# Optimization experiments

Measured on AMD Instinct MI355X. Metric: run time of the kernel, lower is better.

Reference implementation:

```python
import jax, jax.numpy as jnp
from jax import lax
import numpy as np

N = 262144   # occupied voxels
C = 128      # channels
D = 96
K = 27       # 3x3x3 kernel offsets


def _build_kernel_map():
    """Random sparse voxel set + per-offset neighbor indices (Minkowski kernel map)."""
    rng = np.random.default_rng(0)
    cand = rng.integers(0, D, size=(4 * N, 3))
    flat = cand[:, 0] * D * D + cand[:, 1] * D + cand[:, 2]
    uniq = np.unique(flat)[:N]  # N unique occupied voxels
    coords = np.stack([uniq // (D * D), (uniq // D) % D, uniq % D], axis=1)
    lookup = np.full(D * D * D, -1, np.int32)
    lookup[uniq] = np.arange(N, dtype=np.int32)
    offs = np.stack(np.meshgrid([-1, 0, 1], [-1, 0, 1], [-1, 0, 1], indexing='ij'), -1).reshape(-1, 3)
    nc = coords[:, None, :] + offs[None, :, :]            # [N,27,3]
    inb = np.all((nc >= 0) & (nc < D), axis=-1)           # in-bounds
    ncc = np.clip(nc, 0, D - 1)
    nflat = ncc[..., 0] * D * D + ncc[..., 1] * D + ncc[..., 2]
    nid = lookup[nflat]
    mask = inb & (nid >= 0)
    nbr = np.where(mask, nid, 0).astype(np.int32)
    return jnp.asarray(nbr), jnp.asarray(mask)


def setup_inputs() -> dict:
    nbr, mask = _build_kernel_map()
    key = jax.random.key(0)
    ks = jax.random.split(key, 7)
    C4, C2 = C // 4, C // 2
    s3 = lambda cin: 1.0 / np.sqrt(K * cin)
    s1 = lambda cin: 1.0 / np.sqrt(cin)
    return {
        'x':   jax.random.normal(ks[0], (N, C), jnp.float32),
        'nbr': nbr,
        'mask': mask,
        'W00': jax.random.normal(ks[1], (K, C, C4), jnp.float32) * s3(C),
        'b00': jnp.zeros((C4,), jnp.float32),
        'W01': jax.random.normal(ks[2], (K, C4, C2), jnp.float32) * s3(C4),
        'b01': jnp.zeros((C2,), jnp.float32),
        'W10': jax.random.normal(ks[3], (C, C4), jnp.float32) * s1(C),
        'b10': jnp.zeros((C4,), jnp.float32),
        'W11': jax.random.normal(ks[4], (K, C4, C4), jnp.float32) * s3(C4),
        'b11': jnp.zeros((C4,), jnp.float32),
        'W12': jax.random.normal(ks[5], (C4, C2), jnp.float32) * s1(C4),
        'b12': jnp.zeros((C2,), jnp.float32),
    }


def _sparse_conv3(x, W, b, nbr_t, mask_t):
    """Minkowski 3x3x3 stride-1 conv: gather-GEMM-accumulate per kernel offset.
    x: [N,Cin], W: [27,Cin,Cout], nbr_t/mask_t: [27,N]."""
    acc0 = jnp.zeros((x.shape[0], W.shape[-1]), x.dtype)
    def step(acc, kin):
        Wk, idx, m = kin
        return acc + (x[idx] * m[:, None]) @ Wk, None
    y, _ = lax.scan(step, acc0, (W, nbr_t, mask_t))
    return y + b


def reference(x, nbr, mask, W00, b00, W01, b01, W10, b10, W11, b11, W12, b12):
    nbr_t = nbr.T                       # [27,N]
    mask_t = mask.T.astype(x.dtype)     # [27,N]
    # branch 0: conv3x3 -> relu -> conv3x3
    t = jax.nn.relu(_sparse_conv3(x, W00, b00, nbr_t, mask_t))
    out0 = _sparse_conv3(t, W01, b01, nbr_t, mask_t)
    # branch 1: conv1x1 -> relu -> conv3x3 -> relu -> conv1x1
    u = jax.nn.relu(x @ W10 + b10)
    u = jax.nn.relu(_sparse_conv3(u, W11, b11, nbr_t, mask_t))
    out1 = u @ W12 + b12
    # ME.cat(out0, out1) + x  (features concat on channel dim, residual add)
    return jnp.concatenate([out0, out1], axis=1) + x
```

## Files before the change

kernel.cpp:

```cpp
#include <hip/hip_runtime.h>
#include <stdint.h>

#define NVOX 262144
#define CIN  128
#define KOFF 27

typedef short        bf16x8 __attribute__((ext_vector_type(8)));
typedef float        f32x4  __attribute__((ext_vector_type(4)));
typedef int          i32x4  __attribute__((ext_vector_type(4)));
typedef unsigned int u32x4  __attribute__((ext_vector_type(4)));

__device__ __forceinline__ unsigned short f2bf(float x) {
    unsigned int u = __builtin_bit_cast(unsigned int, x);
    u += 0x7fff + ((u >> 16) & 1);
    return (unsigned short)(u >> 16);
}

__global__ void k_detect(const int* __restrict__ mask_i32, int* __restrict__ flag) {
    bool ok = true;
    for (int i = threadIdx.x; i < 256; i += 64) {
        int v = mask_i32[i];
        ok = ok && (v == 0 || v == 1);
    }
    unsigned long long b = __ballot(ok);
    if (threadIdx.x == 0) *flag = (b == ~0ull) ? 1 : 0;
}

__device__ __forceinline__ void pack_one(const float* __restrict__ W,
                                         unsigned short* __restrict__ out,
                                         int K, int Nc, int idx) {
    int j    = idx & 7;
    int lane = (idx >> 3) & 63;
    int f    = idx >> 9;
    int ntiles = Nc >> 4, kcs = K >> 5;
    int g  = f / (kcs * ntiles);
    int rem = f - g * (kcs * ntiles);
    int kc = rem / ntiles;
    int nt = rem - kc * ntiles;
    int k  = kc * 32 + ((lane >> 4) << 3) + j;
    int n  = nt * 16 + (lane & 15);
    out[idx] = f2bf(W[((size_t)g * K + k) * Nc + n]);
}

#define PREP_R0 6912
#define PREP_R1 23296
#define PREP_GRID 24076

__global__ __launch_bounds__(256) void k_prep(
    const int* __restrict__ nbr, const void* __restrict__ mask,
    const int* __restrict__ flag, int* __restrict__ nbr_eff,
    const float* __restrict__ x, u32x4* __restrict__ xb,
    const float* __restrict__ W00, const float* __restrict__ W10,
    const float* __restrict__ W01, const float* __restrict__ W11,
    const float* __restrict__ W12,
    unsigned short* __restrict__ w00p, unsigned short* __restrict__ w10p,
    unsigned short* __restrict__ w01p, unsigned short* __restrict__ w11p,
    unsigned short* __restrict__ w12p)
{
    int b = blockIdx.x, tid = threadIdx.x;
    if (b < PREP_R0) {
        int base = (b * 256 + tid) * 4;
        i32x4 nv = *(const i32x4*)(nbr + base);
        i32x4 r;
        if (*flag) {
            i32x4 mv = *(const i32x4*)((const int*)mask + base);
            r.x = mv.x ? nv.x : -1;
            r.y = mv.y ? nv.y : -1;
            r.z = mv.z ? nv.z : -1;
            r.w = mv.w ? nv.w : -1;
        } else {
            uchar4 mv = *(const uchar4*)((const unsigned char*)mask + base);
            r.x = mv.x ? nv.x : -1;
            r.y = mv.y ? nv.y : -1;
            r.z = mv.z ? nv.z : -1;
            r.w = mv.w ? nv.w : -1;
        }
        *(i32x4*)(nbr_eff + base) = r;
    } else if (b < PREP_R1) {
        int i = (b - PREP_R0) * 256 + tid;
        const float4* p = (const float4*)x + (size_t)i * 2;
        float4 a = p[0], c = p[1];
        uint4 r;
        r.x = f2bf(a.x) | ((unsigned)f2bf(a.y) << 16);
        r.y = f2bf(a.z) | ((unsigned)f2bf(a.w) << 16);
        r.z = f2bf(c.x) | ((unsigned)f2bf(c.y) << 16);
        r.w = f2bf(c.z) | ((unsigned)f2bf(c.w) << 16);
        ((uint4*)xb)[i] = r;
    } else {
        int idx = (b - PREP_R1) * 256 + tid;
        if      (idx < 110592) pack_one(W00, w00p, 128, 32, idx);
        else if (idx < 114688) pack_one(W10, w10p, 128, 32, idx - 110592);
        else if (idx < 169984) pack_one(W01, w01p,  32, 64, idx - 114688);
        else if (idx < 197632) pack_one(W11, w11p,  32, 32, idx - 169984);
        else                   pack_one(W12, w12p,  32, 64, idx - 197632);
    }
}

__global__ __launch_bounds__(256) void k_convA(
    const unsigned short* __restrict__ xb,
    const int* __restrict__ nbr_eff,
    const unsigned short* __restrict__ w00, const unsigned short* __restrict__ w10,
    const float* __restrict__ b00, const float* __restrict__ b10,
    unsigned short* __restrict__ s_out)
{
    __shared__ alignas(16) unsigned char shraw[18432];
    int*            nbr_s = (int*)shraw;
    unsigned short* stage = (unsigned short*)shraw;

    int tid = threadIdx.x;
    int lb = ((blockIdx.x & 7) << 8) | (blockIdx.x >> 3);
    int vb = lb * 128;
    {
        const i32x4* nsrc = (const i32x4*)(nbr_eff + (size_t)vb * 27);
        for (int i = tid; i < 864; i += 256)
            ((i32x4*)nbr_s)[i] = __builtin_nontemporal_load(nsrc + i);
    }
    __syncthreads();

    int lane = tid & 63, wave = tid >> 6;
    int m = lane & 15, q = lane >> 4;
    int vl0 = wave * 32 + m, vl1 = vl0 + 16;

    const bf16x8 zero = {0,0,0,0,0,0,0,0};
    f32x4 zz = {0.f,0.f,0.f,0.f};
    f32x4 t00 = zz, t01 = zz, t10 = zz, t11 = zz;
    f32x4 u00 = zz, u01 = zz, u10 = zz, u11 = zz;

#pragma unroll
    for (int ko = 0; ko < 27; ++ko) {
        int j0 = nbr_s[vl0 * 27 + ko];
        int j1 = nbr_s[vl1 * 27 + ko];
        bool m0 = j0 >= 0, m1 = j1 >= 0;
        const bf16x8* xr0 = (const bf16x8*)(xb + (size_t)(m0 ? j0 : 0) * 128 + q * 8);
        const bf16x8* xr1 = (const bf16x8*)(xb + (size_t)(m1 ? j1 : 0) * 128 + q * 8);
        bf16x8 a0[4], a1[4];
#pragma unroll
        for (int kc = 0; kc < 4; ++kc) {
            a0[kc] = m0 ? xr0[kc * 4] : zero;
            a1[kc] = m1 ? xr1[kc * 4] : zero;
        }
        const bf16x8* wp = (const bf16x8*)(w00) + (size_t)ko * 8 * 64 + lane;
        __builtin_amdgcn_s_setprio(1);
#pragma unroll
        for (int kc = 0; kc < 4; ++kc) {
            bf16x8 bb0 = wp[kc * 128];
            bf16x8 bb1 = wp[kc * 128 + 64];
            t00 = __builtin_amdgcn_mfma_f32_16x16x32_bf16(a0[kc], bb0, t00, 0, 0, 0);
            t01 = __builtin_amdgcn_mfma_f32_16x16x32_bf16(a0[kc], bb1, t01, 0, 0, 0);
            t10 = __builtin_amdgcn_mfma_f32_16x16x32_bf16(a1[kc], bb0, t10, 0, 0, 0);
            t11 = __builtin_amdgcn_mfma_f32_16x16x32_bf16(a1[kc], bb1, t11, 0, 0, 0);
        }
        __builtin_amdgcn_s_setprio(0);
        if (ko == 13) {
            const bf16x8* wq = (const bf16x8*)(w10) + lane;
            __builtin_amdgcn_s_setprio(1);
#pragma unroll
            for (int kc = 0; kc < 4; ++kc) {
                bf16x8 c0 = wq[kc * 128];
                bf16x8 c1 = wq[kc * 128 + 64];
                u00 = __builtin_amdgcn_mfma_f32_16x16x32_bf16(a0[kc], c0, u00, 0, 0, 0);
                u01 = __builtin_amdgcn_mfma_f32_16x16x32_bf16(a0[kc], c1, u01, 0, 0, 0);
                u10 = __builtin_amdgcn_mfma_f32_16x16x32_bf16(a1[kc], c0, u10, 0, 0, 0);
                u11 = __builtin_amdgcn_mfma_f32_16x16x32_bf16(a1[kc], c1, u11, 0, 0, 0);
            }
            __builtin_amdgcn_s_setprio(0);
        }
    }

    __syncthreads();

    int col = lane & 15;
    float bt0 = b00[col], bt1 = b00[16 + col];
    float bu0 = b10[col], bu1 = b10[16 + col];
#pragma unroll
    for (int r = 0; r < 4; ++r) {
        int row0 = wave * 32 + q * 4 + r;
        unsigned short* sp0 = stage + row0 * 72;
        sp0[col]      = f2bf(fmaxf(t00[r] + bt0, 0.f));
        sp0[16 + col] = f2bf(fmaxf(t01[r] + bt1, 0.f));
        sp0[32 + col] = f2bf(fmaxf(u00[r] + bu0, 0.f));
        sp0[48 + col] = f2bf(fmaxf(u01[r] + bu1, 0.f));
        unsigned short* sp1 = sp0 + 16 * 72;
        sp1[col]      = f2bf(fmaxf(t10[r] + bt0, 0.f));
        sp1[16 + col] = f2bf(fmaxf(t11[r] + bt1, 0.f));
        sp1[32 + col] = f2bf(fmaxf(u10[r] + bu0, 0.f));
        sp1[48 + col] = f2bf(fmaxf(u11[r] + bu1, 0.f));
    }
    __syncthreads();
    uint4* g4 = (uint4*)(s_out + (size_t)vb * 64);
    for (int i = tid; i < 1024; i += 256) {
        int row = i >> 3, c = i & 7;
        g4[row * 8 + c] = *(const uint4*)(stage + row * 72 + c * 8);
    }
}

__global__ __launch_bounds__(256) void k_convB(
    const unsigned short* __restrict__ s_in,
    const float* __restrict__ x,
    const int* __restrict__ nbr_eff,
    const unsigned short* __restrict__ w01, const unsigned short* __restrict__ w11,
    const unsigned short* __restrict__ w12,
    const float* __restrict__ b01, const float* __restrict__ b11,
    const float* __restrict__ b12,
    float* __restrict__ out)
{
    __shared__ alignas(16) int nbr_s[128 * 27];
    __shared__ unsigned short vstage[4][2][16 * 40];

    int tid = threadIdx.x;
    int lb = ((blockIdx.x & 7) << 8) | (blockIdx.x >> 3);
    int vb = lb * 128;
    {
        const i32x4* nsrc = (const i32x4*)(nbr_eff + (size_t)vb * 27);
        for (int i = tid; i < 864; i += 256)
            ((i32x4*)nbr_s)[i] = __builtin_nontemporal_load(nsrc + i);
    }
    __syncthreads();

    int lane = tid & 63, wave = tid >> 6;
    int m = lane & 15, q = lane >> 4;
    int vl0 = wave * 32 + m, vl1 = vl0 + 16;

    const bf16x8 zero = {0,0,0,0,0,0,0,0};
    f32x4 zz = {0.f,0.f,0.f,0.f};
    f32x4 o[2][4];
    f32x4 v[2][2];
#pragma unroll
    for (int tl = 0; tl < 2; ++tl) {
        o[tl][0] = zz; o[tl][1] = zz; o[tl][2] = zz; o[tl][3] = zz;
        v[tl][0] = zz; v[tl][1] = zz;
    }

#pragma unroll
    for (int ko = 0; ko < 27; ++ko) {
        int j0 = nbr_s[vl0 * 27 + ko];
        int j1 = nbr_s[vl1 * 27 + ko];
        bool m0 = j0 >= 0, m1 = j1 >= 0;
        const bf16x8* sr0 = (const bf16x8*)(s_in + (size_t)(m0 ? j0 : 0) * 64 + q * 8);
        const bf16x8* sr1 = (const bf16x8*)(s_in + (size_t)(m1 ? j1 : 0) * 64 + q * 8);
        bf16x8 at0 = m0 ? sr0[0] : zero;
        bf16x8 au0 = m0 ? sr0[4] : zero;
        bf16x8 at1 = m1 ? sr1[0] : zero;
        bf16x8 au1 = m1 ? sr1[4] : zero;
        const bf16x8* wp1 = (const bf16x8*)(w01) + (size_t)ko * 4 * 64 + lane;
        __builtin_amdgcn_s_setprio(1);
#pragma unroll
        for (int nt = 0; nt < 4; ++nt) {
            bf16x8 bb = wp1[nt * 64];
            o[0][nt] = __builtin_amdgcn_mfma_f32_16x16x32_bf16(at0, bb, o[0][nt], 0, 0, 0);
            o[1][nt] = __builtin_amdgcn_mfma_f32_16x16x32_bf16(at1, bb, o[1][nt], 0, 0, 0);
        }
        const bf16x8* wp2 = (const bf16x8*)(w11) + (size_t)ko * 2 * 64 + lane;
#pragma unroll
        for (int nt = 0; nt < 2; ++nt) {
            bf16x8 bb = wp2[nt * 64];
            v[0][nt] = __builtin_amdgcn_mfma_f32_16x16x32_bf16(au0, bb, v[0][nt], 0, 0, 0);
            v[1][nt] = __builtin_amdgcn_mfma_f32_16x16x32_bf16(au1, bb, v[1][nt], 0, 0, 0);
        }
        __builtin_amdgcn_s_setprio(0);
    }

    int col = lane & 15;
    {
        float bv0 = b11[col], bv1 = b11[16 + col];
#pragma unroll
        for (int tl = 0; tl < 2; ++tl) {
            unsigned short* vs = vstage[wave][tl];
#pragma unroll
            for (int r = 0; r < 4; ++r) {
                int row = q * 4 + r;
                vs[row * 40 + col]      = f2bf(fmaxf(v[tl][0][r] + bv0, 0.f));
                vs[row * 40 + 16 + col] = f2bf(fmaxf(v[tl][1][r] + bv1, 0.f));
            }
        }
    }
    __syncthreads();
    const bf16x8* wp3 = (const bf16x8*)(w12) + lane;
    bf16x8 w3[4];
#pragma unroll
    for (int nt = 0; nt < 4; ++nt) w3[nt] = wp3[nt * 64];
    f32x4 p[2][4];
#pragma unroll
    for (int tl = 0; tl < 2; ++tl) {
        bf16x8 av = *(const bf16x8*)(vstage[wave][tl] + m * 40 + q * 8);
#pragma unroll
        for (int nt = 0; nt < 4; ++nt)
            p[tl][nt] = __builtin_amdgcn_mfma_f32_16x16x32_bf16(av, w3[nt], zz, 0, 0, 0);
    }

    float bo[4], bp[4];
#pragma unroll
    for (int nt = 0; nt < 4; ++nt) { bo[nt] = b01[nt * 16 + col]; bp[nt] = b12[nt * 16 + col]; }
#pragma unroll
    for (int tl = 0; tl < 2; ++tl) {
#pragma unroll
        for (int r = 0; r < 4; ++r) {
            int row = vb + wave * 32 + tl * 16 + q * 4 + r;
            const float* xr = x + (size_t)row * 128;
            float* orow = out + (size_t)row * 128;
#pragma unroll
            for (int nt = 0; nt < 4; ++nt) {
                float x0 = __builtin_nontemporal_load(xr + nt * 16 + col);
                float x1 = __builtin_nontemporal_load(xr + 64 + nt * 16 + col);
                __builtin_nontemporal_store(o[tl][nt][r] + bo[nt] + x0,
                                            orow + nt * 16 + col);
                __builtin_nontemporal_store(p[tl][nt][r] + bp[nt] + x1,
                                            orow + 64 + nt * 16 + col);
            }
        }
    }
}

extern "C" void kernel_launch(void* const* d_in, const int* in_sizes, int n_in,
                              void* d_out, int out_size, void* d_ws, size_t ws_size,
                              hipStream_t stream) {
    const float* x   = (const float*)d_in[0];
    const int*   nbr = (const int*)d_in[1];
    const void*  mask = d_in[2];
    const float* W00 = (const float*)d_in[3];
    const float* b00 = (const float*)d_in[4];
    const float* W01 = (const float*)d_in[5];
    const float* b01 = (const float*)d_in[6];
    const float* W10 = (const float*)d_in[7];
    const float* b10 = (const float*)d_in[8];
    const float* W11 = (const float*)d_in[9];
    const float* b11 = (const float*)d_in[10];
    const float* W12 = (const float*)d_in[11];
    const float* b12 = (const float*)d_in[12];
    float* out = (float*)d_out;

    char* ws = (char*)d_ws;
    unsigned short* xb     = (unsigned short*)(ws);
    unsigned short* s      = (unsigned short*)(ws + 67108864);
    int*            nbr_eff= (int*)           (ws + 100663296);
    unsigned short* w00p   = (unsigned short*)(ws + 128974848);
    unsigned short* w10p   = (unsigned short*)(ws + 129196032);
    unsigned short* w01p   = (unsigned short*)(ws + 129204224);
    unsigned short* w11p   = (unsigned short*)(ws + 129314816);
    unsigned short* w12p   = (unsigned short*)(ws + 129370112);
    int*            flag   = (int*)           (ws + 129374208);

    k_detect<<<1, 64, 0, stream>>>((const int*)mask, flag);
    k_prep<<<PREP_GRID, 256, 0, stream>>>(nbr, mask, flag, nbr_eff, x, (u32x4*)xb,
                                          W00, W10, W01, W11, W12,
                                          w00p, w10p, w01p, w11p, w12p);
    k_convA<<<NVOX/128, 256, 0, stream>>>(xb, nbr_eff, w00p, w10p, b00, b10, s);
    k_convB<<<NVOX/128, 256, 0, stream>>>(s, x, nbr_eff, w01p, w11p, w12p,
                                          b01, b11, b12, out);
}
```

Before: 649.6 us.

## Double-buffer per-offset conv weights in LDS for both sparse conv kernels

Both conv kernels now stage the weight slice for each kernel offset into shared memory. The next offset's slice is prefetched into registers while the current offset's MFMAs run, then written to the alternate buffer. This replaces per-lane global weight loads with LDS reads and aims to hide weight-fetch latency behind the gather. In exchange it adds a block-wide barrier per offset (27 per block) and raises shared-memory usage, which may lower occupancy.

```diff
diff --git a/kernel.cpp b/kernel.cpp
--- a/kernel.cpp
+++ b/kernel.cpp
@@ -103,8 +103,9 @@
     const float* __restrict__ b00, const float* __restrict__ b10,
     unsigned short* __restrict__ s_out)
 {
-    __shared__ alignas(16) unsigned char shraw[18432];
+    __shared__ alignas(16) unsigned char shraw[30208];
     int*            nbr_s = (int*)shraw;
+    unsigned short* wbuf  = (unsigned short*)(shraw + 13824);
     unsigned short* stage = (unsigned short*)shraw;
 
     int tid = threadIdx.x;
@@ -114,6 +115,12 @@
         const i32x4* nsrc = (const i32x4*)(nbr_eff + (size_t)vb * 27);
         for (int i = tid; i < 864; i += 256)
             ((i32x4*)nbr_s)[i] = __builtin_nontemporal_load(nsrc + i);
+    }
+    {
+        const uint4* g = (const uint4*)w00;
+        uint4 p0 = g[tid], p1 = g[tid + 256];
+        ((uint4*)wbuf)[tid] = p0;
+        ((uint4*)wbuf)[tid + 256] = p1;
     }
     __syncthreads();
 
@@ -128,6 +135,12 @@
 
 #pragma unroll
     for (int ko = 0; ko < 27; ++ko) {
+        const unsigned short* cur = wbuf + (ko & 1) * 4096;
+        uint4 nf0, nf1;
+        if (ko < 26) {
+            const uint4* g = (const uint4*)(w00 + (size_t)(ko + 1) * 4096);
+            nf0 = g[tid]; nf1 = g[tid + 256];
+        }
         int j0 = nbr_s[vl0 * 27 + ko];
         int j1 = nbr_s[vl1 * 27 + ko];
         bool m0 = j0 >= 0, m1 = j1 >= 0;
@@ -139,7 +152,7 @@
             a0[kc] = m0 ? xr0[kc * 4] : zero;
             a1[kc] = m1 ? xr1[kc * 4] : zero;
         }
-        const bf16x8* wp = (const bf16x8*)(w00) + (size_t)ko * 8 * 64 + lane;
+        const bf16x8* wp = (const bf16x8*)cur + lane;
         __builtin_amdgcn_s_setprio(1);
 #pragma unroll
         for (int kc = 0; kc < 4; ++kc) {
@@ -165,9 +178,13 @@
             }
             __builtin_amdgcn_s_setprio(0);
         }
-    }
-
-    __syncthreads();
+        if (ko < 26) {
+            unsigned short* nxt = wbuf + ((ko + 1) & 1) * 4096;
+            ((uint4*)nxt)[tid] = nf0;
+            ((uint4*)nxt)[tid + 256] = nf1;
+        }
+        __syncthreads();
+    }
 
     int col = lane & 15;
     float bt0 = b00[col], bt1 = b00[16 + col];
@@ -204,8 +221,10 @@
     const float* __restrict__ b12,
     float* __restrict__ out)
 {
-    __shared__ alignas(16) int nbr_s[128 * 27];
-    __shared__ unsigned short vstage[4][2][16 * 40];
+    __shared__ alignas(16) unsigned char shraw[26112];
+    int*            nbr_s  = (int*)shraw;
+    unsigned short* wbufB  = (unsigned short*)(shraw + 13824);
+    unsigned short* vstage = (unsigned short*)shraw;
 
     int tid = threadIdx.x;
     int lb = ((blockIdx.x & 7) << 8) | (blockIdx.x >> 3);
@@ -214,6 +233,14 @@
         const i32x4* nsrc = (const i32x4*)(nbr_eff + (size_t)vb * 27);
         for (int i = tid; i < 864; i += 256)
             ((i32x4*)nbr_s)[i] = __builtin_nontemporal_load(nsrc + i);
+    }
+    {
+        uint4 p0 = ((const uint4*)w01)[tid];
+        ((uint4*)wbufB)[tid] = p0;
+        if (tid < 128) {
+            uint4 p1 = ((const uint4*)w11)[tid];
+            ((uint4*)(wbufB + 2048))[tid] = p1;
+        }
     }
     __syncthreads();
 
@@ -233,6 +260,13 @@
 
 #pragma unroll
     for (int ko = 0; ko < 27; ++ko) {
+        const unsigned short* cur = wbufB + (ko & 1) * 3072;
+        uint4 nf0, nf1;
+        if (ko < 26) {
+            nf0 = ((const uint4*)(w01 + (size_t)(ko + 1) * 2048))[tid];
+            if (tid < 128)
+                nf1 = ((const uint4*)(w11 + (size_t)(ko + 1) * 1024))[tid];
+        }
         int j0 = nbr_s[vl0 * 27 + ko];
         int j1 = nbr_s[vl1 * 27 + ko];
         bool m0 = j0 >= 0, m1 = j1 >= 0;
@@ -242,7 +276,8 @@
         bf16x8 au0 = m0 ? sr0[4] : zero;
         bf16x8 at1 = m1 ? sr1[0] : zero;
         bf16x8 au1 = m1 ? sr1[4] : zero;
-        const bf16x8* wp1 = (const bf16x8*)(w01) + (size_t)ko * 4 * 64 + lane;
+        const bf16x8* wp1 = (const bf16x8*)cur + lane;
+        const bf16x8* wp2 = (const bf16x8*)(cur + 2048) + lane;
         __builtin_amdgcn_s_setprio(1);
 #pragma unroll
         for (int nt = 0; nt < 4; ++nt) {
@@ -250,7 +285,6 @@
             o[0][nt] = __builtin_amdgcn_mfma_f32_16x16x32_bf16(at0, bb, o[0][nt], 0, 0, 0);
             o[1][nt] = __builtin_amdgcn_mfma_f32_16x16x32_bf16(at1, bb, o[1][nt], 0, 0, 0);
         }
-        const bf16x8* wp2 = (const bf16x8*)(w11) + (size_t)ko * 2 * 64 + lane;
 #pragma unroll
         for (int nt = 0; nt < 2; ++nt) {
             bf16x8 bb = wp2[nt * 64];
@@ -258,6 +292,12 @@
             v[1][nt] = __builtin_amdgcn_mfma_f32_16x16x32_bf16(au1, bb, v[1][nt], 0, 0, 0);
         }
         __builtin_amdgcn_s_setprio(0);
+        if (ko < 26) {
+            unsigned short* nxt = wbufB + ((ko + 1) & 1) * 3072;
+            ((uint4*)nxt)[tid] = nf0;
+            if (tid < 128) ((uint4*)(nxt + 2048))[tid] = nf1;
+        }
+        __syncthreads();
     }
 
     int col = lane & 15;
@@ -265,7 +305,7 @@
         float bv0 = b11[col], bv1 = b11[16 + col];
 #pragma unroll
         for (int tl = 0; tl < 2; ++tl) {
-            unsigned short* vs = vstage[wave][tl];
+            unsigned short* vs = vstage + (wave * 2 + tl) * 640;
 #pragma unroll
             for (int r = 0; r < 4; ++r) {
                 int row = q * 4 + r;
@@ -274,7 +314,6 @@
             }
         }
     }
-    __syncthreads();
     const bf16x8* wp3 = (const bf16x8*)(w12) + lane;
     bf16x8 w3[4];
 #pragma unroll
@@ -282,7 +321,7 @@
     f32x4 p[2][4];
 #pragma unroll
     for (int tl = 0; tl < 2; ++tl) {
-        bf16x8 av = *(const bf16x8*)(vstage[wave][tl] + m * 40 + q * 8);
+        bf16x8 av = *(const bf16x8*)(vstage + (wave * 2 + tl) * 640 + m * 40 + q * 8);
 #pragma unroll
         for (int nt = 0; nt < 4; ++nt)
             p[tl][nt] = __builtin_amdgcn_mfma_f32_16x16x32_bf16(av, w3[nt], zz, 0, 0, 0);
```

New measurement: 578.9 us. 1.12x faster.
